# Kernel optimization log

Hardware: AMD Instinct MI355X
Metric: run time of the kernel (lower is better)

The kernel has to match this reference:

```python
import jax, jax.numpy as jnp
import numpy as np
from jax import lax

B, N, S, K = 16, 8192, 1024, 32
FACTOR = 1.0
EPS_BN = 1e-5


def farthest_point_sample(xyz, npoint):
    # xyz: [B, N, 3] -> idx [B, npoint]. Deterministic start at index 0
    # (torch version starts at a random index; start choice doesn't change the math pattern).
    b, n, _ = xyz.shape
    bidx = jnp.arange(b)

    def step(carry, _):
        distance, farthest = carry
        centroid = xyz[bidx, farthest]                      # [B, 3]
        dist = jnp.sum((xyz - centroid[:, None, :]) ** 2, -1)  # [B, N]
        distance = jnp.minimum(distance, dist)
        new_far = jnp.argmax(distance, axis=-1)
        return (distance, new_far), farthest

    init = (jnp.full((b, n), 1e10, xyz.dtype), jnp.zeros((b,), jnp.int32))
    _, idxs = lax.scan(step, init, None, length=npoint)
    return idxs.T  # [B, npoint]


def square_distance(src, dst):
    # [B,Ns,3] x [B,Nd,3] -> [B,Ns,Nd]
    d = -2.0 * jnp.einsum('bnc,bmc->bnm', src, dst)
    d += jnp.sum(src ** 2, -1)[:, :, None]
    d += jnp.sum(dst ** 2, -1)[:, None, :]
    return d


def safe_cdist(x):
    # x: [B, C, S]; pairwise euclidean over rows -> [B, C, C]; zero-safe sqrt
    diff = x[:, :, None, :] - x[:, None, :, :]          # [B, C, C, S]
    sq = jnp.sum(diff * diff, -1)
    pos = sq > 0
    return jnp.where(pos, jnp.sqrt(jnp.where(pos, sq, 1.0)), 0.0)


def batchnorm(x, gamma, beta, axes):
    mean = jnp.mean(x, axes, keepdims=True)
    var = jnp.var(x, axes, keepdims=True)  # biased, as in torch BN normalization
    return (x - mean) / jnp.sqrt(var + EPS_BN) * gamma + beta


def reference(xyz, bn1_gamma, bn1_beta, bn2_gamma, bn2_beta):
    b = xyz.shape[0]
    # --- FPS sampling ---
    fps_idx = farthest_point_sample(lax.stop_gradient(xyz), S)          # [B,S]
    new_xyz = jnp.take_along_axis(xyz, fps_idx[:, :, None], axis=1)     # [B,S,3]
    # --- kNN grouping ---
    sq = square_distance(lax.stop_gradient(new_xyz), lax.stop_gradient(xyz))  # [B,S,N]
    _, knn_idx = lax.top_k(-sq, K)                                      # [B,S,K] indices
    grouped = jax.vmap(lambda p, i: p[i])(xyz, knn_idx)                 # [B,S,K,3]
    diff = grouped - new_xyz[:, :, None, :]
    std = jnp.std(diff, ddof=1)                                         # scalar, unbiased like torch.std
    knn_norm = diff / (std + 1e-5)
    center = jnp.broadcast_to(new_xyz[:, :, None, :], (b, S, K, 3))
    knn_xyz = jnp.concatenate([knn_norm, center], axis=-1)              # [B,S,K,6]
    # --- Pooling over neighbors ---
    x = jnp.transpose(knn_xyz, (0, 3, 1, 2))                            # [B,6,S,K]
    lc = jnp.max(x, -1) + jnp.mean(x, -1)                               # [B,6,S]
    lc = jax.nn.relu(batchnorm(lc, bn1_gamma[None, :, None], bn1_beta[None, :, None], (0, 2)))
    # --- Consecutive representation (cdist + superdiagonal factor) ---
    tfcw = safe_cdist(lc)                                               # [B,6,6]
    i = jnp.arange(5)
    tfcw = tfcw.at[:, i, i + 1].multiply(FACTOR)
    # --- Pooling2 ---
    feat = tfcw.reshape(b, -1)                                          # [B,36]
    feat = jax.nn.relu(batchnorm(feat, bn2_gamma[None, :], bn2_beta[None, :], (0,)))
    return feat


def setup_inputs() -> dict:
    key = jax.random.key(0)
    k1, = jax.random.split(key, 1)
    return {
        'xyz': jax.random.normal(k1, (B, N, 3), dtype=jnp.float32),
        'bn1_gamma': jnp.ones((6,), jnp.float32),
        'bn1_beta': jnp.zeros((6,), jnp.float32),
        'bn2_gamma': jnp.ones((36,), jnp.float32),
        'bn2_beta': jnp.zeros((36,), jnp.float32),
    }
```

## Files before the change

### kernel.cpp

```cpp
#include <hip/hip_runtime.h>
#include <hip/hip_bf16.h>

constexpr int BB = 16;
constexpr int NN = 8192;
constexpr int SS = 1024;
constexpr int KK = 32;
constexpr int BUFC = 256;

__device__ __forceinline__ float b2f(__hip_bfloat16 h) { return __bfloat162float(h); }

__device__ __forceinline__ unsigned mkey32(float d) {
    unsigned u = __float_as_uint(d);
    return u ^ (0x80000000u | (unsigned)((int)u >> 31));
}

__device__ __forceinline__ unsigned long long dist_key(const float* __restrict__ pb,
                                                       int idx, float qx, float qy,
                                                       float qz, float qq) {
    float px = pb[idx * 3 + 0];
    float py = pb[idx * 3 + 1];
    float pz = pb[idx * 3 + 2];
    float dot = __fadd_rn(__fadd_rn(__fmul_rn(qx, px), __fmul_rn(qy, py)), __fmul_rn(qz, pz));
    float pp  = __fadd_rn(__fadd_rn(__fmul_rn(px, px), __fmul_rn(py, py)), __fmul_rn(pz, pz));
    float d = __fadd_rn(__fadd_rn(__fmul_rn(-2.0f, dot), qq), pp);
    return ((unsigned long long)mkey32(d) << 32) | (unsigned)idx;
}

template <int CTRL, int RMASK>
__device__ __forceinline__ unsigned long long dppmove_u64(unsigned long long v) {
    int lo = (int)(unsigned)v, hi = (int)(unsigned)(v >> 32);
    int nlo = __builtin_amdgcn_update_dpp(lo, lo, CTRL, RMASK, 0xf, false);
    int nhi = __builtin_amdgcn_update_dpp(hi, hi, CTRL, RMASK, 0xf, false);
    return ((unsigned long long)(unsigned)nhi << 32) | (unsigned)nlo;
}

template <int CTRL, int RMASK>
__device__ __forceinline__ double dppmax_f64(double v) {
    double m = __longlong_as_double(
        dppmove_u64<CTRL, RMASK>((unsigned long long)__double_as_longlong(v)));
    return fmax(v, m);
}

__device__ __forceinline__ double wave_max_dpp_f64(double v) {
    v = dppmax_f64<0x121, 0xf>(v);
    v = dppmax_f64<0x122, 0xf>(v);
    v = dppmax_f64<0x124, 0xf>(v);
    v = dppmax_f64<0x128, 0xf>(v);
    v = dppmax_f64<0x142, 0xa>(v);
    v = dppmax_f64<0x143, 0xc>(v);
    return v;
}

__device__ __forceinline__ unsigned long long bitonic64(unsigned long long v, int lane) {
#pragma unroll
    for (int k = 2; k <= 64; k <<= 1) {
#pragma unroll
        for (int j = k >> 1; j > 0; j >>= 1) {
            unsigned long long p = __shfl_xor(v, j);
            bool up = ((lane & k) == 0);
            bool lower = ((lane & j) == 0);
            bool take_min = (up == lower);
            v = take_min ? (p < v ? p : v) : (p > v ? p : v);
        }
    }
    return v;
}

__device__ __forceinline__ unsigned expand3(unsigned v) {
    v &= 0x3FFu;
    v = (v | (v << 16)) & 0x030000FFu;
    v = (v | (v << 8))  & 0x0300F00Fu;
    v = (v | (v << 4))  & 0x030C30C3u;
    v = (v | (v << 2))  & 0x09249249u;
    return v;
}

__global__ __attribute__((amdgpu_flat_work_group_size(512, 512)))
__attribute__((amdgpu_waves_per_eu(2, 2)))
void fps_kernel(const void* __restrict__ xyz_raw, const void* __restrict__ g1r,
                const void* __restrict__ b1r, const void* __restrict__ g2r,
                const void* __restrict__ b2r, float* __restrict__ xyzf,
                float* __restrict__ new_xyz, float* __restrict__ params,
                void* __restrict__ out_raw, int* __restrict__ done) {
    __shared__ float sxyz[NN * 3];
    __shared__ unsigned sortk[NN];
    __shared__ double skey[2][8];
    __shared__ float sred[6][8];
    __shared__ float sbb[6];

    const unsigned short* u = (const unsigned short*)xyz_raw;
    unsigned short sdet = u[2 * (threadIdx.x & 63)];
    int e = (sdet >> 7) & 0xFF;
    unsigned long long mball = __ballot(e >= 100 && e <= 140);
    const bool isbf = __popcll(mball) > 48;

    if (blockIdx.x >= 16) {
        if (blockIdx.x == 16) {
            int t = threadIdx.x;
            if (t < 85) {
                if (t == 84) {
                    params[84] = isbf ? 1.0f : 0.0f;
                } else {
                    const void* src; int off;
                    if (t < 6)       { src = g1r; off = t; }
                    else if (t < 12) { src = b1r; off = t - 6; }
                    else if (t < 48) { src = g2r; off = t - 12; }
                    else             { src = b2r; off = t - 48; }
                    params[t] = isbf ? b2f(((const __hip_bfloat16*)src)[off])
                                     : ((const float*)src)[off];
                }
            }
            if (t >= 128 && t < 192) {
                for (int i = t - 128; i < 576; i += 64) {
                    if (isbf) ((__hip_bfloat16*)out_raw)[i] = __float2bfloat16(1.0f);
                    else      ((float*)out_raw)[i] = 1.0f;
                }
            }
        }
        float a0 = 1.0f + threadIdx.x * 1e-7f, a1 = 1.1f, a2 = 1.2f, a3 = 1.3f;
        const float mql = 1.0000001f, cdl = 1e-9f;
        for (int it = 0; it < 20000; ++it) {
#pragma unroll
            for (int k = 0; k < 16; ++k) {
                a0 = __fmaf_rn(a0, mql, cdl);
                a1 = __fmaf_rn(a1, mql, cdl);
                a2 = __fmaf_rn(a2, mql, cdl);
                a3 = __fmaf_rn(a3, mql, cdl);
            }
            if ((it & 7) == 0) {
                int d = __hip_atomic_load(done, __ATOMIC_RELAXED,
                                          __HIP_MEMORY_SCOPE_AGENT);
                if (d >= 16) break;
            }
        }
        asm volatile("" :: "v"(a0), "v"(a1), "v"(a2), "v"(a3));
        return;
    }

    constexpr int T = 512, P = NN / T;
    const int b = blockIdx.x, t = threadIdx.x;

    {
        float* xout = xyzf + (size_t)b * NN * 3;
        if (isbf) {
            const __hip_bfloat16* p = (const __hip_bfloat16*)xyz_raw + (size_t)b * NN * 3;
            for (int i = t; i < NN * 3; i += T) {
                float v = b2f(p[i]);
                xout[i] = v;
                sxyz[i] = v;
            }
        } else {
            const float* p = (const float*)xyz_raw + (size_t)b * NN * 3;
            for (int i = t; i < NN * 3; i += T) {
                float v = p[i];
                xout[i] = v;
                sxyz[i] = v;
            }
        }
    }
    __syncthreads();

    {
        float mn[3] = {3.4e38f, 3.4e38f, 3.4e38f};
        float mx[3] = {-3.4e38f, -3.4e38f, -3.4e38f};
        for (int j = 0; j < P; j++) {
            int p = t + j * T;
#pragma unroll
            for (int c = 0; c < 3; c++) {
                float v = sxyz[p * 3 + c];
                mn[c] = fminf(mn[c], v);
                mx[c] = fmaxf(mx[c], v);
            }
        }
#pragma unroll
        for (int o = 32; o > 0; o >>= 1) {
#pragma unroll
            for (int c = 0; c < 3; c++) {
                mn[c] = fminf(mn[c], __shfl_xor(mn[c], o));
                mx[c] = fmaxf(mx[c], __shfl_xor(mx[c], o));
            }
        }
        int wv = t >> 6, ln = t & 63;
        if (ln == 0) {
#pragma unroll
            for (int c = 0; c < 3; c++) { sred[c][wv] = mn[c]; sred[3 + c][wv] = mx[c]; }
        }
        __syncthreads();
        if (t < 6) {
            bool ismin = t < 3;
            float v = sred[t][0];
            for (int w = 1; w < 8; w++) v = ismin ? fminf(v, sred[t][w]) : fmaxf(v, sred[t][w]);
            sbb[t] = v;
        }
        __syncthreads();
    }

    {
        float bx = sbb[0], by = sbb[1], bz = sbb[2];
        float qsx = 63.0f / fmaxf(sbb[3] - bx, 1e-9f);
        float qsy = 63.0f / fmaxf(sbb[4] - by, 1e-9f);
        float qsz = 63.0f / fmaxf(sbb[5] - bz, 1e-9f);
        for (int p = t; p < NN; p += T) {
            unsigned qx = (unsigned)min(63, (int)((sxyz[p * 3 + 0] - bx) * qsx));
            unsigned qy = (unsigned)min(63, (int)((sxyz[p * 3 + 1] - by) * qsy));
            unsigned qz = (unsigned)min(63, (int)((sxyz[p * 3 + 2] - bz) * qsz));
            unsigned m = (expand3(qx) << 2) | (expand3(qy) << 1) | expand3(qz);
            sortk[p] = (m << 13) | (unsigned)p;
        }
        __syncthreads();
        for (unsigned k = 2; k <= (unsigned)NN; k <<= 1) {
            for (unsigned j = k >> 1; j > 0; j >>= 1) {
#pragma unroll
                for (int r = 0; r < NN / 2 / T; r++) {
                    unsigned gid = (unsigned)(r * T + t);
                    unsigned i = ((gid & ~(j - 1)) << 1) | (gid & (j - 1));
                    unsigned p2 = i | j;
                    unsigned a = sortk[i], c2 = sortk[p2];
                    bool up = ((i & k) == 0);
                    if ((a > c2) == up) { sortk[i] = c2; sortk[p2] = a; }
                }
                __syncthreads();
            }
        }
    }

    float px[P], py[P], pz[P], ds[P];
    int nidx[P];
    float l0x = 3.4e38f, l0y = 3.4e38f, l0z = 3.4e38f;
    float h0x = -3.4e38f, h0y = -3.4e38f, h0z = -3.4e38f;
    float l1x = 3.4e38f, l1y = 3.4e38f, l1z = 3.4e38f;
    float h1x = -3.4e38f, h1y = -3.4e38f, h1z = -3.4e38f;
#pragma unroll
    for (int j = 0; j < P; j++) {
        unsigned oi = sortk[t * P + j] & 8191u;
        float x = sxyz[oi * 3 + 0];
        float y = sxyz[oi * 3 + 1];
        float z = sxyz[oi * 3 + 2];
        px[j] = x; py[j] = y; pz[j] = z;
        ds[j] = 1e10f;
        nidx[j] = (int)~oi;
        if (j < 8) {
            l0x = fminf(l0x, x); h0x = fmaxf(h0x, x);
            l0y = fminf(l0y, y); h0y = fmaxf(h0y, y);
            l0z = fminf(l0z, z); h0z = fmaxf(h0z, z);
        } else {
            l1x = fminf(l1x, x); h1x = fmaxf(h1x, x);
            l1y = fminf(l1y, y); h1y = fmaxf(h1y, y);
            l1z = fminf(l1z, z); h1z = fmaxf(h1z, z);
        }
    }
    const float lox = fminf(l0x, l1x), loy = fminf(l0y, l1y), loz = fminf(l0z, l1z);
    const float hix = fmaxf(h0x, h1x), hiy = fmaxf(h0y, h1y), hiz = fmaxf(h0z, h1z);

    __syncthreads();
    float* samples = (float*)sortk;

    float cx = sxyz[0], cy = sxyz[1], cz = sxyz[2];
    if (t == 0) { samples[0] = cx; samples[1] = cy; samples[2] = cz; }
    const int wave = t >> 6, lane = t & 63;

    double hk0 = 0.0, hk1 = 0.0;
    float tb0 = 1e10f, tb1 = 1e10f;

    for (int step = 1; step < SS; step++) {
        float ax = fmaxf(fmaxf(__fsub_rn(lox, cx), __fsub_rn(cx, hix)), 0.0f);
        float ay = fmaxf(fmaxf(__fsub_rn(loy, cy), __fsub_rn(cy, hiy)), 0.0f);
        float az = fmaxf(fmaxf(__fsub_rn(loz, cz), __fsub_rn(cz, hiz)), 0.0f);
        float lbdO = ax * ax + ay * ay + az * az;
        if (lbdO * 0.999f < fmaxf(tb0, tb1)) {
            float a0x = fmaxf(fmaxf(__fsub_rn(l0x, cx), __fsub_rn(cx, h0x)), 0.0f);
            float a0y = fmaxf(fmaxf(__fsub_rn(l0y, cy), __fsub_rn(cy, h0y)), 0.0f);
            float a0z = fmaxf(fmaxf(__fsub_rn(l0z, cz), __fsub_rn(cz, h0z)), 0.0f);
            float lbd0 = a0x * a0x + a0y * a0y + a0z * a0z;
            if (lbd0 * 0.999f < tb0) {
                double kk[8];
#pragma unroll
                for (int j = 0; j < 8; j++) {
                    float dx = __fsub_rn(px[j], cx);
                    float dy = __fsub_rn(py[j], cy);
                    float dz = __fsub_rn(pz[j], cz);
                    float d = __fadd_rn(__fadd_rn(__fmul_rn(dx, dx), __fmul_rn(dy, dy)),
                                        __fmul_rn(dz, dz));
                    float mm = fminf(ds[j], d);
                    ds[j] = mm;
                    kk[j] = __hiloint2double(__float_as_int(mm), nidx[j]);
                }
                double m0 = fmax(kk[0], kk[1]), m1 = fmax(kk[2], kk[3]);
                double m2 = fmax(kk[4], kk[5]), m3 = fmax(kk[6], kk[7]);
                hk0 = fmax(fmax(m0, m1), fmax(m2, m3));
                tb0 = __uint_as_float((unsigned)__double2hiint(hk0));
            }
            float a1x = fmaxf(fmaxf(__fsub_rn(l1x, cx), __fsub_rn(cx, h1x)), 0.0f);
            float a1y = fmaxf(fmaxf(__fsub_rn(l1y, cy), __fsub_rn(cy, h1y)), 0.0f);
            float a1z = fmaxf(fmaxf(__fsub_rn(l1z, cz), __fsub_rn(cz, h1z)), 0.0f);
            float lbd1 = a1x * a1x + a1y * a1y + a1z * a1z;
            if (lbd1 * 0.999f < tb1) {
                double kk[8];
#pragma unroll
                for (int j = 0; j < 8; j++) {
                    float dx = __fsub_rn(px[8 + j], cx);
                    float dy = __fsub_rn(py[8 + j], cy);
                    float dz = __fsub_rn(pz[8 + j], cz);
                    float d = __fadd_rn(__fadd_rn(__fmul_rn(dx, dx), __fmul_rn(dy, dy)),
                                        __fmul_rn(dz, dz));
                    float mm = fminf(ds[8 + j], d);
                    ds[8 + j] = mm;
                    kk[j] = __hiloint2double(__float_as_int(mm), nidx[8 + j]);
                }
                double m0 = fmax(kk[0], kk[1]), m1 = fmax(kk[2], kk[3]);
                double m2 = fmax(kk[4], kk[5]), m3 = fmax(kk[6], kk[7]);
                hk1 = fmax(fmax(m0, m1), fmax(m2, m3));
                tb1 = __uint_as_float((unsigned)__double2hiint(hk1));
            }
        }
        double bk = fmax(hk0, hk1);

        double wk = wave_max_dpp_f64(bk);
        const int par = step & 1;
        if (lane == 63) skey[par][wave] = wk;
        __syncthreads();

        double k0 = fmax(skey[par][0], skey[par][1]);
        double k1 = fmax(skey[par][2], skey[par][3]);
        double k2 = fmax(skey[par][4], skey[par][5]);
        double k3 = fmax(skey[par][6], skey[par][7]);
        double bkk = fmax(fmax(k0, k1), fmax(k2, k3));

        unsigned gidx = ~(unsigned)(unsigned long long)__double_as_longlong(bkk);
        cx = sxyz[gidx * 3 + 0];
        cy = sxyz[gidx * 3 + 1];
        cz = sxyz[gidx * 3 + 2];
        if (t == 0) {
            samples[step * 3 + 0] = cx;
            samples[step * 3 + 1] = cy;
            samples[step * 3 + 2] = cz;
        }
    }

    __syncthreads();
    float* o = new_xyz + (size_t)b * SS * 3;
    for (int i = t; i < SS * 3; i += T) o[i] = samples[i];

    if (t == 0) atomicAdd(done, 1);
}

__global__ __launch_bounds__(256, 2) void knn_kernel(const float* __restrict__ xyzf,
                                                     const float* __restrict__ new_xyz,
                                                     float* __restrict__ A,
                                                     double* __restrict__ qstats) {
    __shared__ unsigned long long buf[4][BUFC];
    const int t = threadIdx.x;
    const int lane = t & 63, wv = t >> 6;
    const int w = blockIdx.x * 4 + wv;
    const int b = w >> 10, s = w & 1023;

    const float* q = new_xyz + ((size_t)b * SS + s) * 3;
    float qx = q[0], qy = q[1], qz = q[2];
    float qq = __fadd_rn(__fadd_rn(__fmul_rn(qx, qx), __fmul_rn(qy, qy)), __fmul_rn(qz, qz));

    const float* pb = xyzf + (size_t)b * NN * 3;
    const unsigned long long ltmask = (1ull << lane) - 1ull;

    unsigned long long lmin = ~0ull;
    for (int j = 0; j < 128; j++) {
        unsigned long long key = dist_key(pb, j * 64 + lane, qx, qy, qz, qq);
        lmin = key < lmin ? key : lmin;
    }

    unsigned long long vs = bitonic64(lmin, lane);
    unsigned long long That = __shfl(vs, 31);

    for (int i = lane; i < BUFC; i += 64) buf[wv][i] = ~0ull;
    int base = 0;
    for (int j = 0; j < 128; j++) {
        unsigned long long key = dist_key(pb, j * 64 + lane, qx, qy, qz, qq);
        bool f = key <= That;
        unsigned long long bal = __ballot(f);
        int pos = base + __popcll(bal & ltmask);
        if (f && pos < BUFC) buf[wv][pos] = key;
        base += __popcll(bal);
    }

    if (base > BUFC) {
        unsigned lo = 0, hi = (unsigned)(That >> 32);
        for (int it = 0; it < 32; it++) {
            unsigned mid = lo + ((hi - lo) >> 1);
            int c = 0;
            for (int j = 0; j < 128; j++) {
                unsigned long long key = dist_key(pb, j * 64 + lane, qx, qy, qz, qq);
                c += ((unsigned)(key >> 32) <= mid) ? 1 : 0;
            }
#pragma unroll
            for (int o = 32; o > 0; o >>= 1) c += __shfl_xor(c, o);
            if (c >= 32) hi = mid; else lo = mid + 1;
        }
        That = ((unsigned long long)hi << 32) | 0xFFFFFFFFull;
        for (int i = lane; i < BUFC; i += 64) buf[wv][i] = ~0ull;
        base = 0;
        for (int j = 0; j < 128; j++) {
            unsigned long long key = dist_key(pb, j * 64 + lane, qx, qy, qz, qq);
            bool f = key <= That;
            unsigned long long bal = __ballot(f);
            int pos = base + __popcll(bal & ltmask);
            if (f && pos < BUFC) buf[wv][pos] = key;
            base += __popcll(bal);
        }
        if (base > BUFC) base = BUFC;
    }

    int M = base;
    unsigned long long kept = ~0ull;
    if (M <= 64) {
        unsigned long long v = (lane < M) ? buf[wv][lane] : ~0ull;
        v = bitonic64(v, lane);
        kept = v;
    } else {
        unsigned long long c0 = buf[wv][lane];
        unsigned long long c1 = buf[wv][64 + lane];
        unsigned long long c2 = buf[wv][128 + lane];
        unsigned long long c3 = buf[wv][192 + lane];
        for (int r = 0; r < KK; r++) {
            unsigned long long m01 = c0 < c1 ? c0 : c1;
            unsigned long long m23 = c2 < c3 ? c2 : c3;
            unsigned long long mm = m01 < m23 ? m01 : m23;
#pragma unroll
            for (int o = 32; o > 0; o >>= 1) {
                unsigned long long t2 = __shfl_xor(mm, o);
                mm = t2 < mm ? t2 : mm;
            }
            if (lane == r) kept = mm;
            c0 = (c0 == mm) ? ~0ull : c0;
            c1 = (c1 == mm) ? ~0ull : c1;
            c2 = (c2 == mm) ? ~0ull : c2;
            c3 = (c3 == mm) ? ~0ull : c3;
        }
    }

    bool act = (lane < KK);
    float gx = 0.0f, gy = 0.0f, gz = 0.0f;
    if (act) {
        unsigned nidx = (unsigned)kept;
        gx = pb[nidx * 3 + 0];
        gy = pb[nidx * 3 + 1];
        gz = pb[nidx * 3 + 2];
    }
    float dx = __fsub_rn(gx, qx);
    float dy = __fsub_rn(gy, qy);
    float dz = __fsub_rn(gz, qz);
    float mx = act ? dx : -3.402823466e38f;
    float my = act ? dy : -3.402823466e38f;
    float mz = act ? dz : -3.402823466e38f;
    float sx = act ? dx : 0.0f;
    float sy = act ? dy : 0.0f;
    float sz = act ? dz : 0.0f;
    double s1 = act ? ((double)dx + (double)dy + (double)dz) : 0.0;
    double s2 = act ? ((double)dx * dx + (double)dy * dy + (double)dz * dz) : 0.0;
#pragma unroll
    for (int o = 32; o > 0; o >>= 1) {
        mx = fmaxf(mx, __shfl_xor(mx, o));
        my = fmaxf(my, __shfl_xor(my, o));
        mz = fmaxf(mz, __shfl_xor(mz, o));
        sx += __shfl_xor(sx, o);
        sy += __shfl_xor(sy, o);
        sz += __shfl_xor(sz, o);
        s1 += __shfl_xor(s1, o);
        s2 += __shfl_xor(s2, o);
    }
    if (lane == 0) {
        float* a = A + ((size_t)b * SS + s) * 3;
        a[0] = __fadd_rn(mx, __fmul_rn(sx, 0.03125f));
        a[1] = __fadd_rn(my, __fmul_rn(sy, 0.03125f));
        a[2] = __fadd_rn(mz, __fmul_rn(sz, 0.03125f));
        qstats[2 * w + 0] = s1;
        qstats[2 * w + 1] = s2;
    }
}

__global__ __launch_bounds__(256) void lc_kernel(const float* __restrict__ new_xyz,
                                                 const float* __restrict__ A,
                                                 const double* __restrict__ qstats,
                                                 float* __restrict__ lc,
                                                 double* __restrict__ bn1acc) {
    __shared__ double red[4];
    __shared__ double r1s[4], r2s[4];
    const int b = blockIdx.x / 6, c = blockIdx.x % 6;
    const int t = threadIdx.x;
    int wv = t >> 6, ln = t & 63;

    double a = 0.0, bsum = 0.0;
    for (int i = t; i < BB * SS; i += 256) { a += qstats[2 * i]; bsum += qstats[2 * i + 1]; }
#pragma unroll
    for (int o = 32; o > 0; o >>= 1) { a += __shfl_xor(a, o); bsum += __shfl_xor(bsum, o); }
    if (ln == 0) { r1s[wv] = a; r2s[wv] = bsum; }
    __syncthreads();
    double sd = r1s[0] + r1s[1] + r1s[2] + r1s[3];
    double sq = r2s[0] + r2s[1] + r2s[2] + r2s[3];

    const double n = (double)BB * SS * KK * 3;
    double var = (sq - sd * sd / n) / (n - 1.0);
    float stdv = (float)sqrt(var);
    float denom = __fadd_rn(stdv, 1e-5f);

    double s1 = 0.0, s2 = 0.0;
    for (int r = 0; r < 4; r++) {
        int s = r * 256 + t;
        float v;
        if (c < 3) {
            v = A[((size_t)b * SS + s) * 3 + c] / denom;
        } else {
            float ww = new_xyz[((size_t)b * SS + s) * 3 + (c - 3)];
            v = __fadd_rn(ww, ww);
        }
        lc[((size_t)b * 6 + c) * SS + s] = v;
        s1 += (double)v;
        s2 += (double)v * (double)v;
    }
#pragma unroll
    for (int off = 32; off > 0; off >>= 1) { s1 += __shfl_down(s1, off); s2 += __shfl_down(s2, off); }
    if (ln == 0) red[wv] = s1;
    __syncthreads();
    if (t == 0) atomicAdd(&bn1acc[c * 2 + 0], red[0] + red[1] + red[2] + red[3]);
    __syncthreads();
    if (ln == 0) red[wv] = s2;
    __syncthreads();
    if (t == 0) atomicAdd(&bn1acc[c * 2 + 1], red[0] + red[1] + red[2] + red[3]);
}

__global__ __launch_bounds__(256) void cdist_kernel(const float* __restrict__ lc,
                                                    const double* __restrict__ bn1acc,
                                                    const float* __restrict__ params,
                                                    float* __restrict__ tf,
                                                    void* __restrict__ out_raw,
                                                    int* __restrict__ cnt) {
    __shared__ float sy[6 * SS];
    __shared__ int lastf;
    const int b = blockIdx.x, t = threadIdx.x;
    float mean[6], sde[6], gg[6], bt[6];
    const double n = (double)BB * SS;
#pragma unroll
    for (int c = 0; c < 6; c++) {
        double m = bn1acc[c * 2 + 0] / n;
        double v = bn1acc[c * 2 + 1] / n - m * m;
        mean[c] = (float)m;
        sde[c] = sqrtf((float)v + 1e-5f);
        gg[c] = params[c];
        bt[c] = params[6 + c];
    }
    for (int r = 0; r < 24; r++) {
        int g = r * 256 + t;
        int c = g >> 10;
        float v = lc[(size_t)b * 6 * SS + g];
        float y = (v - mean[c]) / sde[c] * gg[c] + bt[c];
        sy[g] = fmaxf(y, 0.0f);
    }
    __syncthreads();
    if (t < 6) tf[b * 36 + t * 7] = 0.0f;

    const int w = t >> 6, lane = t & 63;
    const int PI[15] = {0,0,0,0,0,1,1,1,1,2,2,2,3,3,4};
    const int PJ[15] = {1,2,3,4,5,2,3,4,5,3,4,5,4,5,5};
    for (int r = 0; r < 4; r++) {
        int p = w + r * 4;
        if (p < 15) {
            int i = PI[p], j = PJ[p];
            float acc = 0.0f;
            for (int m2 = 0; m2 < 16; m2++) {
                int s = lane + m2 * 64;
                float d = sy[i * SS + s] - sy[j * SS + s];
                acc += d * d;
            }
#pragma unroll
            for (int off = 32; off > 0; off >>= 1) acc += __shfl_down(acc, off);
            if (lane == 0) {
                float v = acc > 0.0f ? sqrtf(acc) : 0.0f;
                const float FACTOR = 1.0f;
                tf[b * 36 + i * 6 + j] = (j == i + 1) ? v * FACTOR : v;
                tf[b * 36 + j * 6 + i] = v;
            }
        }
    }

    __syncthreads();
    __threadfence();
    __syncthreads();
    if (t == 0) { lastf = (atomicAdd(cnt, 1) == BB - 1) ? 1 : 0; }
    __syncthreads();
    if (lastf) {
        __threadfence();
        if (t < 36) {
            int f = t;
            bool isbf = params[84] != 0.0f;
            float x[16]; float sum = 0.0f;
#pragma unroll
            for (int bb2 = 0; bb2 < 16; bb2++) { x[bb2] = tf[bb2 * 36 + f]; sum += x[bb2]; }
            float mean2 = sum * 0.0625f;
            float vs = 0.0f;
#pragma unroll
            for (int bb2 = 0; bb2 < 16; bb2++) { float d = x[bb2] - mean2; vs += d * d; }
            float var2 = vs * 0.0625f;
            float denom2 = sqrtf(var2 + 1e-5f);
            float g = params[12 + f], bb = params[48 + f];
#pragma unroll
            for (int bb2 = 0; bb2 < 16; bb2++) {
                float y = (x[bb2] - mean2) / denom2 * g + bb;
                y = fmaxf(y, 0.0f);
                if (isbf) ((__hip_bfloat16*)out_raw)[bb2 * 36 + f] = __float2bfloat16(y);
                else      ((float*)out_raw)[bb2 * 36 + f] = y;
            }
        }
    }
}

extern "C" void kernel_launch(void* const* d_in, const int* in_sizes, int n_in,
                              void* d_out, int out_size, void* d_ws, size_t ws_size,
                              hipStream_t stream) {
    const void* xyz_raw = d_in[0];
    const void* g1r = d_in[1]; const void* b1r = d_in[2];
    const void* g2r = d_in[3]; const void* b2r = d_in[4];
    {
        const void* six[2] = {nullptr, nullptr}; int n6 = 0;
        const void* t36[2] = {nullptr, nullptr}; int n36 = 0;
        const void* big = nullptr;
        for (int i = 0; i < n_in; i++) {
            if (in_sizes[i] == BB * NN * 3) big = d_in[i];
            else if (in_sizes[i] == 6  && n6  < 2) six[n6++]  = d_in[i];
            else if (in_sizes[i] == 36 && n36 < 2) t36[n36++] = d_in[i];
        }
        if (big && n6 == 2 && n36 == 2) {
            xyz_raw = big; g1r = six[0]; b1r = six[1]; g2r = t36[0]; b2r = t36[1];
        }
    }

    char* ws = (char*)d_ws;
    float* xyzf    = (float*)(ws + 0);
    float* new_xyz = (float*)(ws + 1572864);
    float* A       = (float*)(ws + 1769472);
    float* lc      = (float*)(ws + 1966080);
    float* tf      = (float*)(ws + 2359296);
    double* stats  = (double*)(ws + 2361600);
    double* bn1acc = stats + 2;
    float* params  = (float*)(ws + 2361712);
    int* done      = (int*)(ws + 2362056);
    double* qstats = (double*)(ws + 2362112);

    hipMemsetAsync(stats, 0, 14 * sizeof(double), stream);
    hipMemsetAsync(done, 0, 2 * sizeof(int), stream);
    hipLaunchKernelGGL(fps_kernel, dim3(256), dim3(512), 0, stream,
                       xyz_raw, g1r, b1r, g2r, b2r, xyzf, new_xyz, params, d_out, done);
    hipLaunchKernelGGL(knn_kernel,   dim3(4096), dim3(256), 0, stream, xyzf, new_xyz, A, qstats);
    hipLaunchKernelGGL(lc_kernel,    dim3(96),   dim3(256), 0, stream, new_xyz, A, qstats, lc, bn1acc);
    hipLaunchKernelGGL(cdist_kernel, dim3(16),   dim3(256), 0, stream, lc, bn1acc, params, tf,
                       d_out, done + 1);

    (void)in_sizes; (void)n_in; (void)out_size; (void)ws_size;
}
```

Measured before the change: 1.104 ms.

## Fuse kNN queries into FPS kernel's idle blocks with progress-flag pipelining

Removes the separate kNN kernel. The 240 extra blocks of the FPS launch, which previously only spun, now process kNN queries as soon as the FPS block for that batch has published the sample. FPS blocks write samples straight to global memory and publish progress every 64 steps through release atomics, while consumers poll with acquire loads and sleep between polls. This lets kNN overlap the serial FPS loop. The risks are contention with FPS on the same CUs, a bounded-spin fallback that could read unpublished data if it times out, and ctrl aliasing the lc buffer region.

```diff
diff --git a/kernel.cpp b/kernel.cpp
--- a/kernel.cpp
+++ b/kernel.cpp
@@ -6,6 +6,7 @@
 constexpr int SS = 1024;
 constexpr int KK = 32;
 constexpr int BUFC = 256;
+constexpr int NWORKW = 240 * 8;
 
 __device__ __forceinline__ float b2f(__hip_bfloat16 h) { return __bfloat162float(h); }
 
@@ -75,13 +76,142 @@
     return v;
 }
 
+__device__ void knn_query(const float* __restrict__ xyzf,
+                          const float* __restrict__ new_xyz,
+                          float* __restrict__ A, double* __restrict__ qstats,
+                          int b, int s, int lane,
+                          unsigned long long* __restrict__ buf) {
+    const int w = (b << 10) | s;
+    const float* q = new_xyz + ((size_t)b * SS + s) * 3;
+    float qx = q[0], qy = q[1], qz = q[2];
+    float qq = __fadd_rn(__fadd_rn(__fmul_rn(qx, qx), __fmul_rn(qy, qy)), __fmul_rn(qz, qz));
+
+    const float* pb = xyzf + (size_t)b * NN * 3;
+    const unsigned long long ltmask = (1ull << lane) - 1ull;
+
+    unsigned long long lmin = ~0ull;
+    for (int j = 0; j < 128; j++) {
+        unsigned long long key = dist_key(pb, j * 64 + lane, qx, qy, qz, qq);
+        lmin = key < lmin ? key : lmin;
+    }
+
+    unsigned long long vs = bitonic64(lmin, lane);
+    unsigned long long That = __shfl(vs, 31);
+
+    for (int i = lane; i < BUFC; i += 64) buf[i] = ~0ull;
+    int base = 0;
+    for (int j = 0; j < 128; j++) {
+        unsigned long long key = dist_key(pb, j * 64 + lane, qx, qy, qz, qq);
+        bool f = key <= That;
+        unsigned long long bal = __ballot(f);
+        int pos = base + __popcll(bal & ltmask);
+        if (f && pos < BUFC) buf[pos] = key;
+        base += __popcll(bal);
+    }
+
+    if (base > BUFC) {
+        unsigned lo = 0, hi = (unsigned)(That >> 32);
+        for (int it = 0; it < 32; it++) {
+            unsigned mid = lo + ((hi - lo) >> 1);
+            int c = 0;
+            for (int j = 0; j < 128; j++) {
+                unsigned long long key = dist_key(pb, j * 64 + lane, qx, qy, qz, qq);
+                c += ((unsigned)(key >> 32) <= mid) ? 1 : 0;
+            }
+#pragma unroll
+            for (int o = 32; o > 0; o >>= 1) c += __shfl_xor(c, o);
+            if (c >= 32) hi = mid; else lo = mid + 1;
+        }
+        That = ((unsigned long long)hi << 32) | 0xFFFFFFFFull;
+        for (int i = lane; i < BUFC; i += 64) buf[i] = ~0ull;
+        base = 0;
+        for (int j = 0; j < 128; j++) {
+            unsigned long long key = dist_key(pb, j * 64 + lane, qx, qy, qz, qq);
+            bool f = key <= That;
+            unsigned long long bal = __ballot(f);
+            int pos = base + __popcll(bal & ltmask);
+            if (f && pos < BUFC) buf[pos] = key;
+            base += __popcll(bal);
+        }
+        if (base > BUFC) base = BUFC;
+    }
+
+    int M = base;
+    unsigned long long kept = ~0ull;
+    if (M <= 64) {
+        unsigned long long v = (lane < M) ? buf[lane] : ~0ull;
+        v = bitonic64(v, lane);
+        kept = v;
+    } else {
+        unsigned long long c0 = buf[lane];
+        unsigned long long c1 = buf[64 + lane];
+        unsigned long long c2 = buf[128 + lane];
+        unsigned long long c3 = buf[192 + lane];
+        for (int r = 0; r < KK; r++) {
+            unsigned long long m01 = c0 < c1 ? c0 : c1;
+            unsigned long long m23 = c2 < c3 ? c2 : c3;
+            unsigned long long mm = m01 < m23 ? m01 : m23;
+#pragma unroll
+            for (int o = 32; o > 0; o >>= 1) {
+                unsigned long long t2 = __shfl_xor(mm, o);
+                mm = t2 < mm ? t2 : mm;
+            }
+            if (lane == r) kept = mm;
+            c0 = (c0 == mm) ? ~0ull : c0;
+            c1 = (c1 == mm) ? ~0ull : c1;
+            c2 = (c2 == mm) ? ~0ull : c2;
+            c3 = (c3 == mm) ? ~0ull : c3;
+        }
+    }
+
+    bool act = (lane < KK);
+    float gx = 0.0f, gy = 0.0f, gz = 0.0f;
+    if (act) {
+        unsigned nidx = (unsigned)kept;
+        gx = pb[nidx * 3 + 0];
+        gy = pb[nidx * 3 + 1];
+        gz = pb[nidx * 3 + 2];
+    }
+    float dx = __fsub_rn(gx, qx);
+    float dy = __fsub_rn(gy, qy);
+    float dz = __fsub_rn(gz, qz);
+    float mx = act ? dx : -3.402823466e38f;
+    float my = act ? dy : -3.402823466e38f;
+    float mz = act ? dz : -3.402823466e38f;
+    float sx = act ? dx : 0.0f;
+    float sy = act ? dy : 0.0f;
+    float sz = act ? dz : 0.0f;
+    double s1 = act ? ((double)dx + (double)dy + (double)dz) : 0.0;
+    double s2 = act ? ((double)dx * dx + (double)dy * dy + (double)dz * dz) : 0.0;
+#pragma unroll
+    for (int o = 32; o > 0; o >>= 1) {
+        mx = fmaxf(mx, __shfl_xor(mx, o));
+        my = fmaxf(my, __shfl_xor(my, o));
+        mz = fmaxf(mz, __shfl_xor(mz, o));
+        sx += __shfl_xor(sx, o);
+        sy += __shfl_xor(sy, o);
+        sz += __shfl_xor(sz, o);
+        s1 += __shfl_xor(s1, o);
+        s2 += __shfl_xor(s2, o);
+    }
+    if (lane == 0) {
+        float* a = A + ((size_t)b * SS + s) * 3;
+        a[0] = __fadd_rn(mx, __fmul_rn(sx, 0.03125f));
+        a[1] = __fadd_rn(my, __fmul_rn(sy, 0.03125f));
+        a[2] = __fadd_rn(mz, __fmul_rn(sz, 0.03125f));
+        qstats[2 * w + 0] = s1;
+        qstats[2 * w + 1] = s2;
+    }
+}
+
 __global__ __attribute__((amdgpu_flat_work_group_size(512, 512)))
 __attribute__((amdgpu_waves_per_eu(2, 2)))
 void fps_kernel(const void* __restrict__ xyz_raw, const void* __restrict__ g1r,
                 const void* __restrict__ b1r, const void* __restrict__ g2r,
                 const void* __restrict__ b2r, float* __restrict__ xyzf,
                 float* __restrict__ new_xyz, float* __restrict__ params,
-                void* __restrict__ out_raw, int* __restrict__ done) {
+                void* __restrict__ out_raw, int* __restrict__ ctrl,
+                float* __restrict__ A, double* __restrict__ qstats) {
     __shared__ float sxyz[NN * 3];
     __shared__ unsigned sortk[NN];
     __shared__ double skey[2][8];
@@ -117,6 +247,25 @@
                 }
             }
         }
+
+        const int wv = threadIdx.x >> 6, lane = threadIdx.x & 63;
+        const int gw = (blockIdx.x - 16) * 8 + wv;
+        unsigned long long* mybuf = (unsigned long long*)sxyz + (size_t)wv * BUFC;
+
+        for (int q = gw; q < BB * SS; q += NWORKW) {
+            const int s = q >> 4, b = q & 15;
+            for (int p = 0; p < 300000; ++p) {
+                int pr = __hip_atomic_load(ctrl + b, __ATOMIC_ACQUIRE,
+                                           __HIP_MEMORY_SCOPE_AGENT);
+                if (pr >= s + 1) break;
+                __builtin_amdgcn_s_sleep(64);
+            }
+            knn_query(xyzf, new_xyz, A, qstats, b, s, lane, mybuf);
+            if (lane == 0)
+                __hip_atomic_fetch_add(ctrl + 16, 1, __ATOMIC_RELAXED,
+                                       __HIP_MEMORY_SCOPE_AGENT);
+        }
+
         float a0 = 1.0f + threadIdx.x * 1e-7f, a1 = 1.1f, a2 = 1.2f, a3 = 1.3f;
         const float mql = 1.0000001f, cdl = 1e-9f;
         for (int it = 0; it < 20000; ++it) {
@@ -128,9 +277,9 @@
                 a3 = __fmaf_rn(a3, mql, cdl);
             }
             if ((it & 7) == 0) {
-                int d = __hip_atomic_load(done, __ATOMIC_RELAXED,
+                int d = __hip_atomic_load(ctrl + 16, __ATOMIC_RELAXED,
                                           __HIP_MEMORY_SCOPE_AGENT);
-                if (d >= 16) break;
+                if (d >= BB * SS) break;
             }
         }
         asm volatile("" :: "v"(a0), "v"(a1), "v"(a2), "v"(a3));
@@ -252,11 +401,12 @@
     const float lox = fminf(l0x, l1x), loy = fminf(l0y, l1y), loz = fminf(l0z, l1z);
     const float hix = fmaxf(h0x, h1x), hiy = fmaxf(h0y, h1y), hiz = fmaxf(h0z, h1z);
 
-    __syncthreads();
-    float* samples = (float*)sortk;
-
     float cx = sxyz[0], cy = sxyz[1], cz = sxyz[2];
-    if (t == 0) { samples[0] = cx; samples[1] = cy; samples[2] = cz; }
+    float* ob = new_xyz + (size_t)b * SS * 3;
+    if (t == 0) {
+        ob[0] = cx; ob[1] = cy; ob[2] = cz;
+        __hip_atomic_store(ctrl + b, 1, __ATOMIC_RELEASE, __HIP_MEMORY_SCOPE_AGENT);
+    }
     const int wave = t >> 6, lane = t & 63;
 
     double hk0 = 0.0, hk1 = 0.0;
@@ -331,149 +481,17 @@
         cy = sxyz[gidx * 3 + 1];
         cz = sxyz[gidx * 3 + 2];
         if (t == 0) {
-            samples[step * 3 + 0] = cx;
-            samples[step * 3 + 1] = cy;
-            samples[step * 3 + 2] = cz;
-        }
-    }
-
-    __syncthreads();
-    float* o = new_xyz + (size_t)b * SS * 3;
-    for (int i = t; i < SS * 3; i += T) o[i] = samples[i];
-
-    if (t == 0) atomicAdd(done, 1);
-}
-
-__global__ __launch_bounds__(256, 2) void knn_kernel(const float* __restrict__ xyzf,
-                                                     const float* __restrict__ new_xyz,
-                                                     float* __restrict__ A,
-                                                     double* __restrict__ qstats) {
-    __shared__ unsigned long long buf[4][BUFC];
-    const int t = threadIdx.x;
-    const int lane = t & 63, wv = t >> 6;
-    const int w = blockIdx.x * 4 + wv;
-    const int b = w >> 10, s = w & 1023;
-
-    const float* q = new_xyz + ((size_t)b * SS + s) * 3;
-    float qx = q[0], qy = q[1], qz = q[2];
-    float qq = __fadd_rn(__fadd_rn(__fmul_rn(qx, qx), __fmul_rn(qy, qy)), __fmul_rn(qz, qz));
-
-    const float* pb = xyzf + (size_t)b * NN * 3;
-    const unsigned long long ltmask = (1ull << lane) - 1ull;
-
-    unsigned long long lmin = ~0ull;
-    for (int j = 0; j < 128; j++) {
-        unsigned long long key = dist_key(pb, j * 64 + lane, qx, qy, qz, qq);
-        lmin = key < lmin ? key : lmin;
-    }
-
-    unsigned long long vs = bitonic64(lmin, lane);
-    unsigned long long That = __shfl(vs, 31);
-
-    for (int i = lane; i < BUFC; i += 64) buf[wv][i] = ~0ull;
-    int base = 0;
-    for (int j = 0; j < 128; j++) {
-        unsigned long long key = dist_key(pb, j * 64 + lane, qx, qy, qz, qq);
-        bool f = key <= That;
-        unsigned long long bal = __ballot(f);
-        int pos = base + __popcll(bal & ltmask);
-        if (f && pos < BUFC) buf[wv][pos] = key;
-        base += __popcll(bal);
-    }
-
-    if (base > BUFC) {
-        unsigned lo = 0, hi = (unsigned)(That >> 32);
-        for (int it = 0; it < 32; it++) {
-            unsigned mid = lo + ((hi - lo) >> 1);
-            int c = 0;
-            for (int j = 0; j < 128; j++) {
-                unsigned long long key = dist_key(pb, j * 64 + lane, qx, qy, qz, qq);
-                c += ((unsigned)(key >> 32) <= mid) ? 1 : 0;
-            }
-#pragma unroll
-            for (int o = 32; o > 0; o >>= 1) c += __shfl_xor(c, o);
-            if (c >= 32) hi = mid; else lo = mid + 1;
-        }
-        That = ((unsigned long long)hi << 32) | 0xFFFFFFFFull;
-        for (int i = lane; i < BUFC; i += 64) buf[wv][i] = ~0ull;
-        base = 0;
-        for (int j = 0; j < 128; j++) {
-            unsigned long long key = dist_key(pb, j * 64 + lane, qx, qy, qz, qq);
-            bool f = key <= That;
-            unsigned long long bal = __ballot(f);
-            int pos = base + __popcll(bal & ltmask);
-            if (f && pos < BUFC) buf[wv][pos] = key;
-            base += __popcll(bal);
-        }
-        if (base > BUFC) base = BUFC;
-    }
-
-    int M = base;
-    unsigned long long kept = ~0ull;
-    if (M <= 64) {
-        unsigned long long v = (lane < M) ? buf[wv][lane] : ~0ull;
-        v = bitonic64(v, lane);
-        kept = v;
-    } else {
-        unsigned long long c0 = buf[wv][lane];
-        unsigned long long c1 = buf[wv][64 + lane];
-        unsigned long long c2 = buf[wv][128 + lane];
-        unsigned long long c3 = buf[wv][192 + lane];
-        for (int r = 0; r < KK; r++) {
-            unsigned long long m01 = c0 < c1 ? c0 : c1;
-            unsigned long long m23 = c2 < c3 ? c2 : c3;
-            unsigned long long mm = m01 < m23 ? m01 : m23;
-#pragma unroll
-            for (int o = 32; o > 0; o >>= 1) {
-                unsigned long long t2 = __shfl_xor(mm, o);
-                mm = t2 < mm ? t2 : mm;
-            }
-            if (lane == r) kept = mm;
-            c0 = (c0 == mm) ? ~0ull : c0;
-            c1 = (c1 == mm) ? ~0ull : c1;
-            c2 = (c2 == mm) ? ~0ull : c2;
-            c3 = (c3 == mm) ? ~0ull : c3;
-        }
-    }
-
-    bool act = (lane < KK);
-    float gx = 0.0f, gy = 0.0f, gz = 0.0f;
-    if (act) {
-        unsigned nidx = (unsigned)kept;
-        gx = pb[nidx * 3 + 0];
-        gy = pb[nidx * 3 + 1];
-        gz = pb[nidx * 3 + 2];
-    }
-    float dx = __fsub_rn(gx, qx);
-    float dy = __fsub_rn(gy, qy);
-    float dz = __fsub_rn(gz, qz);
-    float mx = act ? dx : -3.402823466e38f;
-    float my = act ? dy : -3.402823466e38f;
-    float mz = act ? dz : -3.402823466e38f;
-    float sx = act ? dx : 0.0f;
-    float sy = act ? dy : 0.0f;
-    float sz = act ? dz : 0.0f;
-    double s1 = act ? ((double)dx + (double)dy + (double)dz) : 0.0;
-    double s2 = act ? ((double)dx * dx + (double)dy * dy + (double)dz * dz) : 0.0;
-#pragma unroll
-    for (int o = 32; o > 0; o >>= 1) {
-        mx = fmaxf(mx, __shfl_xor(mx, o));
-        my = fmaxf(my, __shfl_xor(my, o));
-        mz = fmaxf(mz, __shfl_xor(mz, o));
-        sx += __shfl_xor(sx, o);
-        sy += __shfl_xor(sy, o);
-        sz += __shfl_xor(sz, o);
-        s1 += __shfl_xor(s1, o);
-        s2 += __shfl_xor(s2, o);
-    }
-    if (lane == 0) {
-        float* a = A + ((size_t)b * SS + s) * 3;
-        a[0] = __fadd_rn(mx, __fmul_rn(sx, 0.03125f));
-        a[1] = __fadd_rn(my, __fmul_rn(sy, 0.03125f));
-        a[2] = __fadd_rn(mz, __fmul_rn(sz, 0.03125f));
-        qstats[2 * w + 0] = s1;
-        qstats[2 * w + 1] = s2;
-    }
+            ob[step * 3 + 0] = cx;
+            ob[step * 3 + 1] = cy;
+            ob[step * 3 + 2] = cz;
+            if ((step & 63) == 0)
+                __hip_atomic_store(ctrl + b, step + 1, __ATOMIC_RELEASE,
+                                   __HIP_MEMORY_SCOPE_AGENT);
+        }
+    }
+
+    if (t == 0)
+        __hip_atomic_store(ctrl + b, SS, __ATOMIC_RELEASE, __HIP_MEMORY_SCOPE_AGENT);
 }
 
 __global__ __launch_bounds__(256) void lc_kernel(const float* __restrict__ new_xyz,
@@ -636,6 +654,7 @@
     float* new_xyz = (float*)(ws + 1572864);
     float* A       = (float*)(ws + 1769472);
     float* lc      = (float*)(ws + 1966080);
+    int* ctrl      = (int*)(ws + 1966080);
     float* tf      = (float*)(ws + 2359296);
     double* stats  = (double*)(ws + 2361600);
     double* bn1acc = stats + 2;
@@ -645,9 +664,10 @@
 
     hipMemsetAsync(stats, 0, 14 * sizeof(double), stream);
     hipMemsetAsync(done, 0, 2 * sizeof(int), stream);
+    hipMemsetAsync(ctrl, 0, 17 * sizeof(int), stream);
     hipLaunchKernelGGL(fps_kernel, dim3(256), dim3(512), 0, stream,
-                       xyz_raw, g1r, b1r, g2r, b2r, xyzf, new_xyz, params, d_out, done);
-    hipLaunchKernelGGL(knn_kernel,   dim3(4096), dim3(256), 0, stream, xyzf, new_xyz, A, qstats);
+                       xyz_raw, g1r, b1r, g2r, b2r, xyzf, new_xyz, params, d_out,
+                       ctrl, A, qstats);
     hipLaunchKernelGGL(lc_kernel,    dim3(96),   dim3(256), 0, stream, new_xyz, A, qstats, lc, bn1acc);
     hipLaunchKernelGGL(cdist_kernel, dim3(16),   dim3(256), 0, stream, lc, bn1acc, params, tf,
                        d_out, done + 1);
```

Result: slower. 1.456 ms (+31.8%).
